# Optimization experiments

Measured on AMD Instinct MI355X. Metric: run time of the kernel, lower is better.

## Reference

```python
import jax, jax.numpy as jnp
import numpy as np

N_HEAD = 12


def setup_inputs() -> dict:
    key = jax.random.key(0)
    k1, k2, k3 = jax.random.split(key, 3)
    B, T, C = 4, 1024, 768
    x = jax.random.normal(k1, (B, T, C), dtype=jnp.float32)
    # torch Linear weight is (out,in); we store transposed so y = x @ W
    w_attn = jax.random.normal(k2, (C, 3 * C), dtype=jnp.float32) * (1.0 / np.sqrt(C))
    w_proj = jax.random.normal(k3, (C, C), dtype=jnp.float32) * (1.0 / np.sqrt(C))
    return {"x": x, "w_attn": w_attn, "w_proj": w_proj}


def reference(x, w_attn, w_proj):
    B, T, C = x.shape
    nh = N_HEAD
    hs = C // nh
    b = 0.01

    qkv = (x @ w_attn).reshape(B, T, 3, nh, hs)
    # per-head-dim standardization; torch.std default is unbiased (ddof=1)
    mu = qkv.mean(axis=-1, keepdims=True)
    sd = jnp.std(qkv, axis=-1, ddof=1, keepdims=True)
    qkv = (qkv - mu) / sd

    # time-leading for scan: (T, B, nh, hs)
    q = jnp.transpose(qkv[:, :, 0], (1, 0, 2, 3))
    k = jnp.transpose(qkv[:, :, 1], (1, 0, 2, 3))
    v = jnp.transpose(qkv[:, :, 2], (1, 0, 2, 3))

    eye = jnp.eye(hs, dtype=x.dtype) * 0.99  # hs_eye

    def step(S, qkv_t):
        q_t, k_t, v_t = qkv_t  # each (B, nh, hs)
        # L_t = 0.99*I - b * k k^T ; I_t = k v^T  (computed on the fly, not materialized over T)
        L_t = eye - b * jnp.einsum('bhi,bhj->bhij', k_t, k_t)
        I_t = jnp.einsum('bhi,bhj->bhij', k_t, v_t)
        S = jnp.einsum('bhij,bhjk->bhik', S, L_t) + I_t
        o_t = jnp.einsum('bhj,bhij->bhi', q_t, S)
        return S, o_t

    S0 = jnp.zeros((B, nh, hs, hs), dtype=x.dtype)
    _, vt = jax.lax.scan(step, S0, (q, k, v))  # vt: (T, B, nh, hs)

    y = jnp.transpose(vt, (1, 0, 2, 3)).reshape(B, T, C) @ w_proj
    return x + y
```

## Files before the change

kernel.cpp:

```cpp
#include <hip/hip_runtime.h>

typedef unsigned short u16;
typedef __attribute__((ext_vector_type(4))) unsigned short u16x4;
typedef __attribute__((ext_vector_type(8))) short bf16x8;
typedef __attribute__((ext_vector_type(4))) float f32x4;

#define B_ 4
#define T_ 1024
#define NH 12
#define HS 64
#define CDIM 768
#define QKVW 2304
#define NC 16
#define CS 64
#define LAM 0.99f
#define BP  (0.01f/0.99f)
#define MROWS 4096
#define LSTR 72

#define OFF_WPT 4718592
#define OFF_W  9437184
#define OFF_U  (OFF_W  + 768*4096)
#define OFF_C  (OFF_U  + 768*4096)
#define OFF_R0 (OFF_C  + 768*4096)
#define OFF_XB (OFF_W)
#define OFF_WAT (OFF_W + 1572864)

__device__ __forceinline__ u16 f2bf(float f) {
    union { float f; unsigned u; } a; a.f = f;
    const unsigned r = a.u + 0x7FFF + ((a.u >> 16) & 1);
    return (u16)(r >> 16);
}
__device__ __forceinline__ float bf2f(u16 h) {
    union { unsigned u; float f; } a; a.u = ((unsigned)h) << 16; return a.f;
}
__device__ __forceinline__ u16x4 f2bf4(const f32x4 v) {
    u16x4 u; u.x = f2bf(v[0]); u.y = f2bf(v[1]); u.z = f2bf(v[2]); u.w = f2bf(v[3]);
    return u;
}

__device__ __forceinline__ void tcast_body(const float* __restrict__ src,
                                           u16* __restrict__ dst,
                                           int Cn, int Rr, int bx, int by) {
    const int ln = threadIdx.x & 63, kg = threadIdx.x >> 6;
    const int n = bx * 64 + ln;
    const int kb = by * 64 + kg * 16;
    u16 tmp[16];
#pragma unroll
    for (int j = 0; j < 16; ++j)
        tmp[j] = f2bf(src[(size_t)(kb + j) * Cn + n]);
#pragma unroll
    for (int j4 = 0; j4 < 4; ++j4) {
        u16x4 u; u.x = tmp[j4*4]; u.y = tmp[j4*4+1]; u.z = tmp[j4*4+2]; u.w = tmp[j4*4+3];
        *(u16x4*)&dst[(size_t)n * Rr + kb + j4*4] = u;
    }
}

__global__ __launch_bounds__(256)
void cast_all_kernel(const float* __restrict__ x, const float* __restrict__ wa,
                     const float* __restrict__ wp, u16* __restrict__ xb,
                     u16* __restrict__ waT, u16* __restrict__ wpT) {
    const int bid = blockIdx.x;
    if (bid < 3072) {
        const size_t i = ((size_t)bid * 256 + threadIdx.x) * 4;
        const float4 v = *(const float4*)(x + i);
        u16x4 u;
        u.x = f2bf(v.x); u.y = f2bf(v.y); u.z = f2bf(v.z); u.w = f2bf(v.w);
        *(u16x4*)(xb + i) = u;
    } else if (bid < 3504) {
        const int idx = bid - 3072;
        tcast_body(wa, waT, QKVW, CDIM, idx % 36, idx / 36);
    } else {
        const int idx = bid - 3504;
        tcast_body(wp, wpT, CDIM, CDIM, idx % 12, idx / 12);
    }
}

__device__ __forceinline__ void gll16(const u16* g, u16* lds) {
    __builtin_amdgcn_global_load_lds(
        (const __attribute__((address_space(1))) unsigned*)g,
        (__attribute__((address_space(3))) unsigned*)lds, 16, 0, 0);
}

template<bool ADD_RES, bool NORM>
__global__ __launch_bounds__(256)
void gemm_mfma(const u16* __restrict__ A, const u16* __restrict__ Bt,
               const float* __restrict__ R, void* __restrict__ Cout,
               int N, int K) {
    __shared__ u16 As[128 * 64];
    __shared__ u16 Bs[128 * 64];
    const int tid  = threadIdx.x;
    const int wave = tid >> 6, lane = tid & 63;
    const int wm = wave >> 1, wn = wave & 1;
    const int ln = lane & 15, quad = lane >> 4;
    const int m0 = blockIdx.y * 128, n0 = blockIdx.x * 128;

    const int rl = lane >> 3;
    const int kx = ((lane & 7) ^ rl) * 8;
    const u16* Ag = A + (size_t)(m0 + wave * 32 + rl) * K + kx;
    const u16* Bg = Bt + (size_t)(n0 + wave * 32 + rl) * K + kx;
    u16* AsW = &As[(wave * 32) * 64];
    u16* BsW = &Bs[(wave * 32) * 64];

    f32x4 acc[4][4] = {};

    for (int k0 = 0; k0 < K; k0 += 64) {
        __syncthreads();
#pragma unroll
        for (int c8 = 0; c8 < 4; ++c8) {
            gll16(Ag + (size_t)(c8 * 8) * K + k0, AsW + c8 * 8 * 64);
            gll16(Bg + (size_t)(c8 * 8) * K + k0, BsW + c8 * 8 * 64);
        }
        __syncthreads();
#pragma unroll
        for (int k32 = 0; k32 < 64; k32 += 32) {
            const int ko = (k32 + quad * 8) ^ ((ln & 7) * 8);
            bf16x8 af[4], bfr[4];
#pragma unroll
            for (int mi = 0; mi < 4; ++mi)
                af[mi] = *(const bf16x8*)&As[(wm * 64 + mi * 16 + ln) * 64 + ko];
#pragma unroll
            for (int ni = 0; ni < 4; ++ni)
                bfr[ni] = *(const bf16x8*)&Bs[(wn * 64 + ni * 16 + ln) * 64 + ko];
#pragma unroll
            for (int mi = 0; mi < 4; ++mi)
#pragma unroll
                for (int ni = 0; ni < 4; ++ni)
                    acc[mi][ni] = __builtin_amdgcn_mfma_f32_16x16x32_bf16(
                        af[mi], bfr[ni], acc[mi][ni], 0, 0, 0);
        }
    }

#pragma unroll
    for (int mi = 0; mi < 4; ++mi) {
        const int rb = m0 + wm * 64 + mi * 16 + quad * 4;
#pragma unroll
        for (int r = 0; r < 4; ++r) {
            if (NORM) {
                const float a0 = acc[mi][0][r], a1 = acc[mi][1][r];
                const float a2 = acc[mi][2][r], a3 = acc[mi][3][r];
                float s1 = a0 + a1 + a2 + a3;
                float s2 = a0*a0 + a1*a1 + a2*a2 + a3*a3;
#pragma unroll
                for (int m = 1; m < 16; m <<= 1) {
                    s1 += __shfl_xor(s1, m, 64);
                    s2 += __shfl_xor(s2, m, 64);
                }
                const float mu = s1 * (1.0f / 64.0f);
                const float rs = rsqrtf((s2 - 64.0f * mu * mu) * (1.0f / 63.0f));
                u16* op = (u16*)Cout + (size_t)(rb + r) * N + n0 + wn * 64 + ln;
                op[0]  = f2bf((a0 - mu) * rs);
                op[16] = f2bf((a1 - mu) * rs);
                op[32] = f2bf((a2 - mu) * rs);
                op[48] = f2bf((a3 - mu) * rs);
            } else {
#pragma unroll
                for (int ni = 0; ni < 4; ++ni) {
                    const int col = n0 + wn * 64 + ni * 16 + ln;
                    float v = acc[mi][ni][r];
                    if (ADD_RES) v += R[(size_t)(rb + r) * N + col];
                    ((float*)Cout)[(size_t)(rb + r) * N + col] = v;
                }
            }
        }
    }
}

template<bool ASWZ, bool BSWZ>
__device__ __forceinline__ void mm_strip2(const u16* A, const u16* Bq,
                                          int wr, int ln, int quad, f32x4 (&acc)[4]) {
#pragma unroll
    for (int k0 = 0; k0 < 64; k0 += 32) {
        const int kq = k0 + quad * 8;
        const int ks = kq ^ ((ln & 7) * 8);
        const bf16x8 a = ASWZ ? *(const bf16x8*)&A[(wr + ln) * 64 + ks]
                              : *(const bf16x8*)&A[(wr + ln) * LSTR + kq];
#pragma unroll
        for (int nt = 0; nt < 4; ++nt) {
            const bf16x8 b = BSWZ ? *(const bf16x8*)&Bq[(nt * 16 + ln) * 64 + ks]
                                  : *(const bf16x8*)&Bq[(nt * 16 + ln) * LSTR + kq];
            acc[nt] = __builtin_amdgcn_mfma_f32_16x16x32_bf16(a, b, acc[nt], 0, 0, 0);
        }
    }
}

__global__ __launch_bounds__(256, 3)
void chunkA(const u16* __restrict__ qkv, float* __restrict__ ws,
            u16* __restrict__ wbg, u16* __restrict__ ktg) {
    __shared__ u16 Kb[64 * LSTR], Vb[64 * LSTR], KT[64 * LSTR],
                   VT[64 * LSTR], NT[64 * LSTR];
    u16* const Yb = Kb;
    u16* const Np = Vb;
    u16* const UT = NT;
    u16* const HbT = VT;

    const int cc = blockIdx.x;
    const int bh = cc >> 4, c = cc & 15;
    const int b = bh / NH, h = bh - b * NH;
    const int tid = threadIdx.x;
    const int w = tid >> 6, lane = tid & 63;
    const int ln = lane & 15, quad = lane >> 4;
    const int wr = w * 16;
    const u16* base = qkv + ((size_t)(b * T_ + c * CS)) * QKVW + h * HS;

    {
        const int tr0 = w * 4 + quad;
        const int d0 = ln * 4;
        float vsc = __powf(LAM, -(float)(tr0 + 1));
        const float v16 = __powf(LAM, -16.0f);
#pragma unroll
        for (int p = 0; p < 4; ++p) {
            const int t = p * 16 + tr0;
            const u16x4 k4 = *(const u16x4*)(base + (size_t)t * QKVW + CDIM + d0);
            const u16x4 vu = *(const u16x4*)(base + (size_t)t * QKVW + 2 * CDIM + d0);
            u16x4 v4; v4.x = f2bf(bf2f(vu.x) * vsc); v4.y = f2bf(bf2f(vu.y) * vsc);
            v4.z = f2bf(bf2f(vu.z) * vsc); v4.w = f2bf(bf2f(vu.w) * vsc);
            *(u16x4*)&Kb[t * LSTR + d0] = k4;
            *(u16x4*)&Vb[t * LSTR + d0] = v4;
            KT[(d0 + 0) * LSTR + t] = k4.x; KT[(d0 + 1) * LSTR + t] = k4.y;
            KT[(d0 + 2) * LSTR + t] = k4.z; KT[(d0 + 3) * LSTR + t] = k4.w;
            VT[(d0 + 0) * LSTR + t] = v4.x; VT[(d0 + 1) * LSTR + t] = v4.y;
            VT[(d0 + 2) * LSTR + t] = v4.z; VT[(d0 + 3) * LSTR + t] = v4.w;
            vsc *= v16;
        }
    }
    __syncthreads();

    f32x4 accG[4] = {}, accH[4] = {}, c1[4] = {};
    mm_strip2<false,false>(Kb, Kb, wr, ln, quad, accG);
    mm_strip2<false,false>(Kb, Vb, wr, ln, quad, accH);
    mm_strip2<false,false>(VT, KT, wr, ln, quad, c1);
    __syncthreads();

#pragma unroll
    for (int nt = 0; nt < 4; ++nt) {
        const int col = nt * 16 + ln;
        u16x4 nvT, hvT;
#pragma unroll
        for (int r = 0; r < 4; ++r) {
            const int row = wr + quad * 4 + r;
            const float g = accG[nt][r];
            const u16 nv = (col < row) ? f2bf(BP * g) : (u16)0;
            Np[row * LSTR + col] = nv;
            Yb[row * LSTR + col] = (row == col) ? f2bf(1.0f)
                                 : ((col < row) ? f2bf(-BP * g) : (u16)0);
            ((u16*)&nvT)[r] = nv;
            ((u16*)&hvT)[r] = (col < row) ? f2bf(accH[nt][r]) : (u16)0;
        }
        *(u16x4*)&NT[col * LSTR + wr + quad * 4] = nvT;
        *(u16x4*)&HbT[col * LSTR + wr + quad * 4] = hvT;
    }
    __syncthreads();

    for (int j = 0; j < 3; ++j) {
        f32x4 sq[4] = {};
        mm_strip2<false,false>(Np, NT, wr, ln, quad, sq);
        __syncthreads();
#pragma unroll
        for (int nt = 0; nt < 4; ++nt) {
            const int col = nt * 16 + ln;
            u16x4 sv;
#pragma unroll
            for (int r = 0; r < 4; ++r) {
                const u16 v = f2bf(sq[nt][r]);
                Np[(wr + quad * 4 + r) * LSTR + col] = v;
                ((u16*)&sv)[r] = v;
            }
            *(u16x4*)&NT[col * LSTR + wr + quad * 4] = sv;
        }
        __syncthreads();
        f32x4 ya[4];
#pragma unroll
        for (int nt = 0; nt < 4; ++nt)
#pragma unroll
            for (int r = 0; r < 4; ++r)
                ya[nt][r] = bf2f(Yb[(wr + quad * 4 + r) * LSTR + nt * 16 + ln]);
        mm_strip2<false,false>(Yb, NT, wr, ln, quad, ya);
#pragma unroll
        for (int nt = 0; nt < 4; ++nt)
#pragma unroll
            for (int r = 0; r < 4; ++r)
                Yb[(wr + quad * 4 + r) * LSTR + nt * 16 + ln] = f2bf(ya[nt][r]);
    }

    u16* Ugp = (u16*)(ws + OFF_U) + (size_t)cc * 4096;
    u16* Cgp = (u16*)(ws + OFF_C) + (size_t)cc * 4096;

    f32x4 wv[4] = {};
    mm_strip2<false,false>(Yb, KT, wr, ln, quad, wv);

    f32x4 m1[4] = {};
    mm_strip2<false,false>(Yb, HbT, wr, ln, quad, m1);
#pragma unroll
    for (int nt = 0; nt < 4; ++nt)
#pragma unroll
        for (int r = 0; r < 4; ++r)
            Np[(wr + quad * 4 + r) * LSTR + nt * 16 + ln] = f2bf(m1[nt][r]);

#pragma unroll
    for (int nt = 0; nt < 4; ++nt)
#pragma unroll
        for (int r = 0; r < 4; ++r)
            Yb[(wr + quad * 4 + r) * LSTR + nt * 16 + ln] = f2bf(wv[nt][r]);

    f32x4 uv[4] = {};
    mm_strip2<false,false>(Np, KT, wr, ln, quad, uv);
#pragma unroll
    for (int nt = 0; nt < 4; ++nt)
        *(u16x4*)&Ugp[(size_t)(w * 64 + lane) * 16 + nt * 4] = f2bf4(uv[nt]);
    __syncthreads();
#pragma unroll
    for (int nt = 0; nt < 4; ++nt)
        *(u16x4*)&UT[(nt * 16 + ln) * LSTR + wr + quad * 4] = f2bf4(uv[nt]);
    __syncthreads();

    f32x4 c2[4] = {};
    mm_strip2<false,false>(KT, UT, wr, ln, quad, c2);
#pragma unroll
    for (int nt = 0; nt < 4; ++nt) {
        const f32x4 cv = c1[nt] - BP * c2[nt];
        *(u16x4*)&Cgp[(size_t)(w * 64 + lane) * 16 + nt * 4] = f2bf4(cv);
    }

    for (int e = tid; e < 512; e += 256) {
        const int t = e >> 3, g = e & 7;
        *(bf16x8*)&wbg[(size_t)cc * 4096 + t * 64 + ((g ^ (t & 7)) << 3)] =
            *(const bf16x8*)&Yb[t * LSTR + (g << 3)];
    }
    for (int e = tid; e < 512; e += 256) {
        const int d = e >> 3, g = e & 7;
        *(bf16x8*)&ktg[(size_t)cc * 4096 + d * 64 + ((g ^ (d & 7)) << 3)] =
            *(const bf16x8*)&KT[d * LSTR + (g << 3)];
    }
}

__global__ __launch_bounds__(256)
void chunkB(float* __restrict__ ws, const u16* __restrict__ wbg,
            const u16* __restrict__ ktg) {
    __shared__ u16 WBs[2][4096], KTs[2][4096];
    __shared__ u16 RTb[64 * LSTR], PTb[64 * LSTR];

    const int bh = blockIdx.x;
    const int tid = threadIdx.x;
    const int w = tid >> 6, lane = tid & 63;
    const int ln = lane & 15, quad = lane >> 4;
    const int wr = w * 16;
    const float lam64 = __powf(LAM, 64.0f);
    u16* r0tg = (u16*)(ws + OFF_R0);

    f32x4 R[4] = {};

    for (int e = tid; e < 64 * LSTR; e += 256) RTb[e] = 0;

    const int off = w * 1024;
    {
        const size_t b0 = (size_t)(bh * 16) * 4096;
#pragma unroll
        for (int i = 0; i < 2; ++i) {
            gll16(wbg + b0 + off + i * 512 + lane * 8, &WBs[0][off + i * 512]);
            gll16(ktg + b0 + off + i * 512 + lane * 8, &KTs[0][off + i * 512]);
        }
    }
    __syncthreads();

    for (int c = 0; c < NC; ++c) {
        const int buf = c & 1;
        const size_t cc = (size_t)(bh * 16 + c);

        if (c + 1 < NC) {
            const size_t b1 = (cc + 1) * 4096;
#pragma unroll
            for (int i = 0; i < 2; ++i) {
                gll16(wbg + b1 + off + i * 512 + lane * 8, &WBs[buf ^ 1][off + i * 512]);
                gll16(ktg + b1 + off + i * 512 + lane * 8, &KTs[buf ^ 1][off + i * 512]);
            }
        }

        const u16* Cg = (const u16*)(ws + OFF_C) + cc * 4096
                        + (size_t)(w * 64 + lane) * 16;
        const bf16x8 cu0 = *(const bf16x8*)&Cg[0];
        const bf16x8 cu1 = *(const bf16x8*)&Cg[8];

        f32x4 p[4] = {};
        mm_strip2<true,false>(&WBs[buf][0], RTb, wr, ln, quad, p);
#pragma unroll
        for (int nt = 0; nt < 4; ++nt)
            *(u16x4*)&PTb[(nt * 16 + ln) * LSTR + wr + quad * 4] = f2bf4(p[nt]);
        __syncthreads();

        f32x4 kp[4] = {};
        mm_strip2<true,false>(&KTs[buf][0], PTb, wr, ln, quad, kp);

        u16* r0t = r0tg + cc * 4096;
        const int swz = (wr + quad * 4) ^ ((ln & 7) * 8);
#pragma unroll
        for (int nt = 0; nt < 4; ++nt) {
            const int x = nt * 16 + ln;
            *(u16x4*)&r0t[x * 64 + swz] = f2bf4(R[nt]);
            const bf16x8 cu = (nt < 2) ? cu0 : cu1;
            const int o = (nt & 1) * 4;
            f32x4 cv; cv[0] = bf2f((u16)cu[o + 0]); cv[1] = bf2f((u16)cu[o + 1]);
            cv[2] = bf2f((u16)cu[o + 2]); cv[3] = bf2f((u16)cu[o + 3]);
            R[nt] = lam64 * (R[nt] - BP * kp[nt] + cv);
            *(u16x4*)&RTb[x * LSTR + wr + quad * 4] = f2bf4(R[nt]);
        }
        __syncthreads();
    }
}

__global__ __launch_bounds__(256, 3)
void chunkC(const u16* __restrict__ qkv, float* __restrict__ ws,
            const u16* __restrict__ wbg, const u16* __restrict__ ktg,
            u16* __restrict__ ob) {
    __shared__ u16 Wb[4096], KTb[4096];
    __shared__ u16 RuT[64 * LSTR];
    __shared__ u16 Qhb[64 * LSTR], Kb[64 * LSTR], Vtb[64 * LSTR];
    u16* const R0Tb = RuT;
    u16* const RmTb = RuT;
    u16* const A1m = Kb;
    u16* const A2m = Vtb;

    const int cc = blockIdx.x;
    const int bh = cc >> 4, c = cc & 15;
    const int b = bh / NH, h = bh - b * NH;
    const int tid = threadIdx.x;
    const int w = tid >> 6, lane = tid & 63;
    const int ln = lane & 15, quad = lane >> 4;
    const int wr = w * 16;
    const u16* base = qkv + ((size_t)(b * T_ + c * CS)) * QKVW + h * HS;
    const u16* r0tg = (const u16*)(ws + OFF_R0);

    const int off = w * 1024;
    {
        const size_t bb = (size_t)cc * 4096;
#pragma unroll
        for (int i = 0; i < 2; ++i) {
            gll16(wbg  + bb + off + i * 512 + lane * 8, &Wb[off + i * 512]);
            gll16(ktg  + bb + off + i * 512 + lane * 8, &KTb[off + i * 512]);
            gll16(r0tg + bb + off + i * 512 + lane * 8, &R0Tb[off + i * 512]);
        }
    }
    {
        const int tr0 = w * 4 + quad;
        const int d0 = ln * 4;
        float qsc = __powf(LAM, (float)(tr0 + 1));
        float vsc = 1.0f / qsc;
        const float q16 = __powf(LAM, 16.0f);
        const float v16 = 1.0f / q16;
#pragma unroll
        for (int p = 0; p < 4; ++p) {
            const int t = p * 16 + tr0;
            const u16x4 qu = *(const u16x4*)(base + (size_t)t * QKVW + d0);
            const u16x4 ku = *(const u16x4*)(base + (size_t)t * QKVW + CDIM + d0);
            const u16x4 vu = *(const u16x4*)(base + (size_t)t * QKVW + 2 * CDIM + d0);
            u16x4 q4; q4.x = f2bf(bf2f(qu.x) * qsc); q4.y = f2bf(bf2f(qu.y) * qsc);
            q4.z = f2bf(bf2f(qu.z) * qsc); q4.w = f2bf(bf2f(qu.w) * qsc);
            u16x4 v4; v4.x = f2bf(bf2f(vu.x) * vsc); v4.y = f2bf(bf2f(vu.y) * vsc);
            v4.z = f2bf(bf2f(vu.z) * vsc); v4.w = f2bf(bf2f(vu.w) * vsc);
            *(u16x4*)&Qhb[t * LSTR + d0] = q4;
            *(u16x4*)&Kb[t * LSTR + d0] = ku;
            *(u16x4*)&Vtb[t * LSTR + d0] = v4;
            qsc *= q16; vsc *= v16;
        }
    }
    __syncthreads();

    const u16* Ugp = (const u16*)(ws + OFF_U) + (size_t)cc * 4096
                     + (size_t)(w * 64 + lane) * 16;
    const bf16x8 uu0 = *(const bf16x8*)&Ugp[0];
    const bf16x8 uu1 = *(const bf16x8*)&Ugp[8];

    f32x4 a1[4] = {}, a2[4] = {};
    mm_strip2<false,false>(Qhb, Kb,   wr, ln, quad, a1);
    mm_strip2<false,false>(Qhb, Vtb,  wr, ln, quad, a2);
    __syncthreads();

    const int row = wr + quad * 4;
#pragma unroll
    for (int nt = 0; nt < 4; ++nt) {
        const int col = nt * 16 + ln;
#pragma unroll
        for (int r = 0; r < 4; ++r) {
            const int t = row + r;
            A1m[t * LSTR + col] = (col <= t) ? f2bf(a1[nt][r]) : (u16)0;
            A2m[t * LSTR + col] = (col <= t) ? f2bf(a2[nt][r]) : (u16)0;
        }
    }

    f32x4 Oacc[4] = {}, wr0[4] = {};
    mm_strip2<false,true >(Qhb, R0Tb, wr, ln, quad, Oacc);
    mm_strip2<true ,true >(Wb,  R0Tb, wr, ln, quad, wr0);
#pragma unroll
    for (int nt = 0; nt < 4; ++nt) {
        const bf16x8 uu = (nt < 2) ? uu0 : uu1;
        const int o = (nt & 1) * 4;
        wr0[nt][0] += bf2f((u16)uu[o + 0]); wr0[nt][1] += bf2f((u16)uu[o + 1]);
        wr0[nt][2] += bf2f((u16)uu[o + 2]); wr0[nt][3] += bf2f((u16)uu[o + 3]);
    }
    __syncthreads();

#pragma unroll
    for (int nt = 0; nt < 4; ++nt)
        *(u16x4*)&RmTb[(nt * 16 + ln) * LSTR + row] = f2bf4(wr0[nt]);
    __syncthreads();

    f32x4 O3[4] = {};
    mm_strip2<false,true >(A2m, KTb,  wr, ln, quad, Oacc);
    mm_strip2<false,false>(A1m, RmTb, wr, ln, quad, O3);

#pragma unroll
    for (int nt = 0; nt < 4; ++nt) {
        const int col = nt * 16 + ln;
#pragma unroll
        for (int r = 0; r < 4; ++r) {
            const float o = Oacc[nt][r] - BP * O3[nt][r];
            ob[((size_t)(b * T_ + c * CS + row + r)) * CDIM + h * HS + col] = f2bf(o);
        }
    }
}

extern "C" void kernel_launch(void* const* d_in, const int* in_sizes, int n_in,
                              void* d_out, int out_size, void* d_ws, size_t ws_size,
                              hipStream_t stream) {
    const float* x      = (const float*)d_in[0];
    const float* w_attn = (const float*)d_in[1];
    const float* w_proj = (const float*)d_in[2];
    float* ws  = (float*)d_ws;
    u16* qkv = (u16*)ws;
    u16* xb  = (u16*)(ws + OFF_XB);
    u16* waT = (u16*)(ws + OFF_WAT);
    u16* wpT = (u16*)(ws + OFF_WPT);
    u16* ob  = (u16*)(ws + OFF_C);
    u16* wbg = (u16*)d_out;
    u16* ktg = (u16*)d_out + 768 * 4096;

    cast_all_kernel<<<3648, 256, 0, stream>>>(x, w_attn, w_proj, xb, waT, wpT);

    gemm_mfma<false, true><<<dim3(QKVW / 128, MROWS / 128), 256, 0, stream>>>(
        xb, waT, nullptr, qkv, QKVW, CDIM);

    chunkA<<<768, 256, 0, stream>>>(qkv, ws, wbg, ktg);
    chunkB<<<48,  256, 0, stream>>>(ws, wbg, ktg);
    chunkC<<<768, 256, 0, stream>>>(qkv, ws, wbg, ktg, ob);

    gemm_mfma<true, false><<<dim3(CDIM / 128, MROWS / 128), 256, 0, stream>>>(
        ob, wpT, x, (float*)d_out, CDIM, CDIM);
}
```

Before: 171.1 us.

## Split chunkB recurrence across four column-quarter blocks per head

The sequential inter-chunk state recurrence in chunkB is split so that each (batch, head) gets four blocks, each owning 16 of the 64 state columns. Because the recurrence is linear per column, the quarters evolve independently. This raises the grid from 48 to 192 blocks to fill more CUs on the latency-bound serial kernel. In exchange, every block reloads the full W and K^T tiles, so global and LDS traffic for those operands is quadrupled.

```diff
diff --git a/kernel.cpp b/kernel.cpp
--- a/kernel.cpp
+++ b/kernel.cpp
@@ -166,9 +166,9 @@
     }
 }
 
-template<bool ASWZ, bool BSWZ>
-__device__ __forceinline__ void mm_strip2(const u16* A, const u16* Bq,
-                                          int wr, int ln, int quad, f32x4 (&acc)[4]) {
+template<bool ASWZ, bool BSWZ, int NT>
+__device__ __forceinline__ void mm_stripN(const u16* A, const u16* Bq,
+                                          int wr, int ln, int quad, f32x4 (&acc)[NT]) {
 #pragma unroll
     for (int k0 = 0; k0 < 64; k0 += 32) {
         const int kq = k0 + quad * 8;
@@ -176,12 +176,18 @@
         const bf16x8 a = ASWZ ? *(const bf16x8*)&A[(wr + ln) * 64 + ks]
                               : *(const bf16x8*)&A[(wr + ln) * LSTR + kq];
 #pragma unroll
-        for (int nt = 0; nt < 4; ++nt) {
+        for (int nt = 0; nt < NT; ++nt) {
             const bf16x8 b = BSWZ ? *(const bf16x8*)&Bq[(nt * 16 + ln) * 64 + ks]
                                   : *(const bf16x8*)&Bq[(nt * 16 + ln) * LSTR + kq];
             acc[nt] = __builtin_amdgcn_mfma_f32_16x16x32_bf16(a, b, acc[nt], 0, 0, 0);
         }
     }
+}
+
+template<bool ASWZ, bool BSWZ>
+__device__ __forceinline__ void mm_strip2(const u16* A, const u16* Bq,
+                                          int wr, int ln, int quad, f32x4 (&acc)[4]) {
+    mm_stripN<ASWZ, BSWZ, 4>(A, Bq, wr, ln, quad, acc);
 }
 
 __global__ __launch_bounds__(256, 3)
@@ -338,9 +344,11 @@
 void chunkB(float* __restrict__ ws, const u16* __restrict__ wbg,
             const u16* __restrict__ ktg) {
     __shared__ u16 WBs[2][4096], KTs[2][4096];
-    __shared__ u16 RTb[64 * LSTR], PTb[64 * LSTR];
-
-    const int bh = blockIdx.x;
+    __shared__ u16 RTb[16 * LSTR], PTb[16 * LSTR];
+
+    const int bid = blockIdx.x;
+    const int bh = bid >> 2, qtr = bid & 3;
+    const int cb = qtr * 16;
     const int tid = threadIdx.x;
     const int w = tid >> 6, lane = tid & 63;
     const int ln = lane & 15, quad = lane >> 4;
@@ -348,9 +356,9 @@
     const float lam64 = __powf(LAM, 64.0f);
     u16* r0tg = (u16*)(ws + OFF_R0);
 
-    f32x4 R[4] = {};
-
-    for (int e = tid; e < 64 * LSTR; e += 256) RTb[e] = 0;
+    f32x4 R[1] = {};
+
+    for (int e = tid; e < 16 * LSTR; e += 256) RTb[e] = 0;
 
     const int off = w * 1024;
     {
@@ -377,33 +385,25 @@
         }
 
         const u16* Cg = (const u16*)(ws + OFF_C) + cc * 4096
-                        + (size_t)(w * 64 + lane) * 16;
-        const bf16x8 cu0 = *(const bf16x8*)&Cg[0];
-        const bf16x8 cu1 = *(const bf16x8*)&Cg[8];
-
-        f32x4 p[4] = {};
-        mm_strip2<true,false>(&WBs[buf][0], RTb, wr, ln, quad, p);
-#pragma unroll
-        for (int nt = 0; nt < 4; ++nt)
-            *(u16x4*)&PTb[(nt * 16 + ln) * LSTR + wr + quad * 4] = f2bf4(p[nt]);
+                        + (size_t)(w * 64 + lane) * 16 + qtr * 4;
+        const u16x4 cu = *(const u16x4*)Cg;
+
+        f32x4 p[1] = {};
+        mm_stripN<true,false,1>(&WBs[buf][0], RTb, wr, ln, quad, p);
+        *(u16x4*)&PTb[ln * LSTR + wr + quad * 4] = f2bf4(p[0]);
         __syncthreads();
 
-        f32x4 kp[4] = {};
-        mm_strip2<true,false>(&KTs[buf][0], PTb, wr, ln, quad, kp);
+        f32x4 kp[1] = {};
+        mm_stripN<true,false,1>(&KTs[buf][0], PTb, wr, ln, quad, kp);
 
         u16* r0t = r0tg + cc * 4096;
         const int swz = (wr + quad * 4) ^ ((ln & 7) * 8);
-#pragma unroll
-        for (int nt = 0; nt < 4; ++nt) {
-            const int x = nt * 16 + ln;
-            *(u16x4*)&r0t[x * 64 + swz] = f2bf4(R[nt]);
-            const bf16x8 cu = (nt < 2) ? cu0 : cu1;
-            const int o = (nt & 1) * 4;
-            f32x4 cv; cv[0] = bf2f((u16)cu[o + 0]); cv[1] = bf2f((u16)cu[o + 1]);
-            cv[2] = bf2f((u16)cu[o + 2]); cv[3] = bf2f((u16)cu[o + 3]);
-            R[nt] = lam64 * (R[nt] - BP * kp[nt] + cv);
-            *(u16x4*)&RTb[x * LSTR + wr + quad * 4] = f2bf4(R[nt]);
-        }
+        const int x = cb + ln;
+        *(u16x4*)&r0t[x * 64 + swz] = f2bf4(R[0]);
+        f32x4 cv; cv[0] = bf2f(cu.x); cv[1] = bf2f(cu.y);
+        cv[2] = bf2f(cu.z); cv[3] = bf2f(cu.w);
+        R[0] = lam64 * (R[0] - BP * kp[0] + cv);
+        *(u16x4*)&RTb[ln * LSTR + wr + quad * 4] = f2bf4(R[0]);
         __syncthreads();
     }
 }
@@ -540,7 +540,7 @@
         xb, waT, nullptr, qkv, QKVW, CDIM);
 
     chunkA<<<768, 256, 0, stream>>>(qkv, ws, wbg, ktg);
-    chunkB<<<48,  256, 0, stream>>>(ws, wbg, ktg);
+    chunkB<<<192, 256, 0, stream>>>(ws, wbg, ktg);
     chunkC<<<768, 256, 0, stream>>>(qkv, ws, wbg, ktg, ob);
 
     gemm_mfma<true, false><<<dim3(CDIM / 128, MROWS / 128), 256, 0, stream>>>(
```

New measurement: 164.1 us. -4.1%, faster.
